# Kernel tuning notes

Measured on AMD Instinct MI355X. Metric: run time of the kernel, lower is better.

Reference implementation:

```python
import jax, jax.numpy as jnp
import numpy as np

B, T, D, U = 64, 512, 512, 512


def setup_inputs() -> dict:
    key = jax.random.key(0)
    k1, k2, k3 = jax.random.split(key, 3)
    x = jax.random.normal(k1, (B, T, D), dtype=jnp.float32)
    Wk = jax.random.normal(k2, (D, 4 * U), dtype=jnp.float32) * (1.0 / np.sqrt(D))
    Wr = jax.random.normal(k3, (U, 4 * U), dtype=jnp.float32) * (1.0 / np.sqrt(U))
    # bias init per module: zeros(i), ones(f), zeros(g), zeros(o)
    b = jnp.concatenate([jnp.zeros(U), jnp.ones(U), jnp.zeros(2 * U)]).astype(jnp.float32)
    return {"x": x, "Wk": Wk, "Wr": Wr, "b": b}


def reference(x, Wk, Wr, b):
    units = Wr.shape[0]
    # Precompute input projection for all timesteps in one GEMM (same math).
    zx = jnp.einsum('btd,dk->btk', x, Wk)  # [B, T, 4U]
    h0 = jnp.zeros((x.shape[0], units), dtype=x.dtype)
    c0 = jnp.zeros((x.shape[0], units), dtype=x.dtype)

    def step(carry, zx_t):
        h, c = carry
        z = zx_t + h @ Wr + b  # [B, 4U]
        zi, zf, zg, zo = jnp.split(z, 4, axis=-1)
        i = jax.nn.sigmoid(zi)
        f = jax.nn.sigmoid(zf)
        c_new = f * c + i * jnp.tanh(zg)
        o = jax.nn.sigmoid(zo)
        h_new = o * jnp.tanh(c_new)
        return (h_new, c_new), None

    (h_last, c_last), _ = jax.lax.scan(step, (h0, c0), jnp.swapaxes(zx, 0, 1))
    # default flags: return_sequence=False, return_states=False -> last hidden
    return h_last
```

## Files before the change

### kernel.cpp

```cpp
#include <hip/hip_runtime.h>
#include <hip/hip_bf16.h>
#include <math.h>

#define BSZ 64
#define TT  512
#define DD  512
#define UU  512
#define NZ  2048

#define NSL    32
#define USL    16
#define NBG    4
#define BG     16
#define KSTEPS 16

using short8  = __attribute__((ext_vector_type(8))) short;
using floatx4 = __attribute__((ext_vector_type(4))) float;
typedef unsigned long long u64;

template <bool ZXBF16>
__global__ __launch_bounds__(256) void gemm_zx(const float* __restrict__ A,
                                               const float* __restrict__ B,
                                               void* __restrict__ Cout) {
  __shared__ float As[16][65];
  __shared__ float Bs[16][64];

  const int tid = threadIdx.x;
  const int tx = tid & 15;
  const int ty = tid >> 4;
  const int m0 = blockIdx.y * 64;
  const int n0 = blockIdx.x * 64;

  const int lm  = tid >> 2;
  const int lk4 = (tid & 3) * 4;
  const int lk  = tid >> 4;
  const int ln4 = (tid & 15) * 4;

  float acc[4][4] = {};

  for (int k0 = 0; k0 < DD; k0 += 16) {
    float4 av = *(const float4*)(A + (size_t)(m0 + lm) * DD + k0 + lk4);
    float4 bv = *(const float4*)(B + (size_t)(k0 + lk) * NZ + n0 + ln4);
    As[lk4 + 0][lm] = av.x;
    As[lk4 + 1][lm] = av.y;
    As[lk4 + 2][lm] = av.z;
    As[lk4 + 3][lm] = av.w;
    *(float4*)&Bs[lk][ln4] = bv;
    __syncthreads();
#pragma unroll
    for (int kk = 0; kk < 16; ++kk) {
      float a[4], b[4];
#pragma unroll
      for (int i = 0; i < 4; ++i) a[i] = As[kk][ty * 4 + i];
#pragma unroll
      for (int j = 0; j < 4; ++j) b[j] = Bs[kk][tx * 4 + j];
#pragma unroll
      for (int i = 0; i < 4; ++i)
#pragma unroll
        for (int j = 0; j < 4; ++j) acc[i][j] = fmaf(a[i], b[j], acc[i][j]);
    }
    __syncthreads();
  }

#pragma unroll
  for (int i = 0; i < 4; ++i) {
    const size_t row = (size_t)(m0 + ty * 4 + i) * NZ + n0 + tx * 4;
    if constexpr (ZXBF16) {
      __hip_bfloat16* C = (__hip_bfloat16*)Cout;
#pragma unroll
      for (int j = 0; j < 4; ++j) C[row + j] = __float2bfloat16(acc[i][j]);
    } else {
      float* C = (float*)Cout;
      *(float4*)&C[row] = make_float4(acc[i][0], acc[i][1], acc[i][2], acc[i][3]);
    }
  }
}

__device__ __forceinline__ floatx4 mfma16(short8 a, short8 b, floatx4 c) {
  return __builtin_amdgcn_mfma_f32_16x16x32_bf16(a, b, c, 0, 0, 0);
}

template <bool ZXBF16>
__global__ __launch_bounds__(256) void lstm_persist(
    const void* __restrict__ zx_, const float* __restrict__ Wr,
    const float* __restrict__ bias, unsigned short* __restrict__ h_hi,
    unsigned short* __restrict__ h_lo, int* __restrict__ flags,
    float* __restrict__ out) {
  extern __shared__ char lds[];
  unsigned short* wr_hi = (unsigned short*)lds;
  unsigned short* wr_lo = wr_hi + KSTEPS * 4 * 64 * 8;
  float* z_ex = (float*)(wr_lo + KSTEPS * 4 * 64 * 8);

  const int sl = blockIdx.x;
  const int bg = blockIdx.y;
  const int tid = threadIdx.x;
  const int g = tid >> 6;
  const int lane = tid & 63;
  const int u0 = sl * USL;

  {
    const int cidx = tid & 63;
    const int koff = tid >> 6;
    const int gg = cidx >> 4, u = cidx & 15;
    const int col = gg * UU + u0 + u;
    for (int k0 = 0; k0 < DD; k0 += 4) {
      const int k = k0 + koff;
      const float v = Wr[(size_t)k * NZ + col];
      const __hip_bfloat16 vh = __float2bfloat16(v);
      const float rem = v - __bfloat162float(vh);
      const __hip_bfloat16 vl = __float2bfloat16(rem);
      const int K = k >> 5, kg = (k >> 3) & 3, j = k & 7;
      const int off = ((K * 4 + gg) * 64 + (kg * 16 + u)) * 8 + j;
      wr_hi[off] = *(const unsigned short*)&vh;
      wr_lo[off] = *(const unsigned short*)&vl;
    }
  }
  __syncthreads();

  const int am = lane & 15, akg = lane >> 4;
  const size_t arow = (size_t)(bg * BG + am) * UU + akg * 8;

  const int eb = tid >> 4;
  const int eu = tid & 15;
  const int b = bg * BG + eb;
  const float bias_i = bias[0 * UU + u0 + eu];
  const float bias_f = bias[1 * UU + u0 + eu];
  const float bias_g = bias[2 * UU + u0 + eu];
  const float bias_o = bias[3 * UU + u0 + eu];
  float c_state = 0.f;
  const size_t plane_t = (size_t)BSZ * UU;
  const int wword = (b * UU + u0 + eu) >> 1;

  int* myflag = flags + (bg * NSL + sl) * 16;

  for (int t = 0; t < TT; ++t) {
    float zi, zf, zg, zo;
    {
      const size_t zb = ((size_t)b * TT + t) * NZ + u0 + eu;
      if constexpr (ZXBF16) {
        const unsigned short* zx = (const unsigned short*)zx_;
        zi = __bfloat162float(*(const __hip_bfloat16*)&zx[zb + 0 * UU]);
        zf = __bfloat162float(*(const __hip_bfloat16*)&zx[zb + 1 * UU]);
        zg = __bfloat162float(*(const __hip_bfloat16*)&zx[zb + 2 * UU]);
        zo = __bfloat162float(*(const __hip_bfloat16*)&zx[zb + 3 * UU]);
      } else {
        const float* zx = (const float*)zx_;
        zi = zx[zb + 0 * UU];
        zf = zx[zb + 1 * UU];
        zg = zx[zb + 2 * UU];
        zo = zx[zb + 3 * UU];
      }
    }

    if (tid < NSL) {
      const int* fp = flags + (bg * NSL + tid) * 16;
      while (__hip_atomic_load(fp, __ATOMIC_RELAXED, __HIP_MEMORY_SCOPE_AGENT) < t) {
      }
    }
    __syncthreads();
    __builtin_amdgcn_fence(__ATOMIC_ACQUIRE, "workgroup");

    const unsigned short* Ahi = h_hi + (size_t)t * plane_t + arow;
    const unsigned short* Alo = h_lo + (size_t)t * plane_t + arow;
    floatx4 a0 = {0, 0, 0, 0}, a1 = {0, 0, 0, 0}, a2 = {0, 0, 0, 0};
#pragma unroll 4
    for (int K = 0; K < KSTEPS; ++K) {
      const short8 ahi = *(const short8*)(Ahi + K * 32);
      const short8 alo = *(const short8*)(Alo + K * 32);
      const short8 bhi = *(const short8*)(wr_hi + ((K * 4 + g) * 64 + lane) * 8);
      const short8 blo = *(const short8*)(wr_lo + ((K * 4 + g) * 64 + lane) * 8);
      a0 = mfma16(ahi, bhi, a0);
      a1 = mfma16(ahi, blo, a1);
      a2 = mfma16(alo, bhi, a2);
    }
#pragma unroll
    for (int r = 0; r < 4; ++r) {
      const int bb = (lane >> 4) * 4 + r;
      z_ex[(g * 16 + bb) * 16 + (lane & 15)] = a0[r] + a1[r] + a2[r];
    }
    __syncthreads();

    zi += z_ex[(0 * 16 + eb) * 16 + eu] + bias_i;
    zf += z_ex[(1 * 16 + eb) * 16 + eu] + bias_f;
    zg += z_ex[(2 * 16 + eb) * 16 + eu] + bias_g;
    zo += z_ex[(3 * 16 + eb) * 16 + eu] + bias_o;

    const float ig = 1.f / (1.f + expf(-zi));
    const float fg = 1.f / (1.f + expf(-zf));
    const float gg = tanhf(zg);
    const float og = 1.f / (1.f + expf(-zo));
    c_state = fg * c_state + ig * gg;
    const float hn = og * tanhf(c_state);

    const __hip_bfloat16 hh = __float2bfloat16(hn);
    const float hrem = hn - __bfloat162float(hh);
    const __hip_bfloat16 hl = __float2bfloat16(hrem);
    const unsigned int vhi = (unsigned int)*(const unsigned short*)&hh;
    const unsigned int vlo = (unsigned int)*(const unsigned short*)&hl;
    const unsigned int phi_n = (unsigned int)__shfl_xor((int)vhi, 1);
    const unsigned int plo_n = (unsigned int)__shfl_xor((int)vlo, 1);
    if ((tid & 1) == 0) {
      const unsigned int whi = vhi | (phi_n << 16);
      const unsigned int wlo = vlo | (plo_n << 16);
      unsigned int* phi = (unsigned int*)(h_hi + (size_t)(t + 1) * plane_t) + wword;
      unsigned int* plo = (unsigned int*)(h_lo + (size_t)(t + 1) * plane_t) + wword;
      __hip_atomic_store(phi, whi, __ATOMIC_RELAXED, __HIP_MEMORY_SCOPE_AGENT);
      __hip_atomic_store(plo, wlo, __ATOMIC_RELAXED, __HIP_MEMORY_SCOPE_AGENT);
    }

    if (t == TT - 1) out[(size_t)b * UU + u0 + eu] = hn;

    __syncthreads();
    if (tid == 0)
      __hip_atomic_store(myflag, t + 1, __ATOMIC_RELAXED,
                         __HIP_MEMORY_SCOPE_AGENT);
  }
}

extern "C" void kernel_launch(void* const* d_in, const int* in_sizes, int n_in,
                              void* d_out, int out_size, void* d_ws, size_t ws_size,
                              hipStream_t stream) {
  const float* x    = (const float*)d_in[0];
  const float* Wk   = (const float*)d_in[1];
  const float* Wr   = (const float*)d_in[2];
  const float* bias = (const float*)d_in[3];
  float* out = (float*)d_out;

  const size_t plane_t = (size_t)BSZ * UU;
  const size_t hplane_bytes = (size_t)(TT + 1) * plane_t * 2;
  const size_t flags_bytes = (size_t)NBG * NSL * 16 * 4;
  const size_t zx_f32_bytes = (size_t)BSZ * TT * NZ * 4;

  const size_t need_f32 = zx_f32_bytes + 2 * hplane_bytes + flags_bytes;
  const bool use_bf16_zx = (ws_size < need_f32);
  const size_t zx_bytes = use_bf16_zx ? zx_f32_bytes / 2 : zx_f32_bytes;

  char* ws = (char*)d_ws;
  void* zx = (void*)ws;
  unsigned short* h_hi = (unsigned short*)(ws + zx_bytes);
  unsigned short* h_lo = (unsigned short*)(ws + zx_bytes + hplane_bytes);
  int* flags = (int*)(ws + zx_bytes + 2 * hplane_bytes);

  hipMemsetAsync(h_hi, 0, plane_t * 2, stream);
  hipMemsetAsync(h_lo, 0, plane_t * 2, stream);
  hipMemsetAsync(flags, 0, flags_bytes, stream);

  dim3 ggrid(NZ / 64, (BSZ * TT) / 64);
  if (use_bf16_zx)
    gemm_zx<true><<<ggrid, 256, 0, stream>>>(x, Wk, zx);
  else
    gemm_zx<false><<<ggrid, 256, 0, stream>>>(x, Wk, zx);

  const int lds_bytes = KSTEPS * 4 * 64 * 8 * 2 * 2 + 4 * 16 * 16 * 4;
  dim3 pgrid(NSL, NBG);
  if (use_bf16_zx) {
    hipFuncSetAttribute(reinterpret_cast<const void*>(lstm_persist<true>),
                        hipFuncAttributeMaxDynamicSharedMemorySize, lds_bytes);
    lstm_persist<true><<<pgrid, 256, lds_bytes, stream>>>(zx, Wr, bias, h_hi, h_lo,
                                                          flags, out);
  } else {
    hipFuncSetAttribute(reinterpret_cast<const void*>(lstm_persist<false>),
                        hipFuncAttributeMaxDynamicSharedMemorySize, lds_bytes);
    lstm_persist<false><<<pgrid, 256, lds_bytes, stream>>>(zx, Wr, bias, h_hi, h_lo,
                                                           flags, out);
  }
}
```

Before: 4.406 ms.

## Pin LSTM batch groups to XCDs via runtime election, use plain stores locally

Splits the batch into 8 groups of 8 rows and grows the persistent grid to 256 blocks. Each block reads its hardware XCC_ID and joins an atomic election that assigns it a batch group on its own XCD, so each batch group's hidden-state exchange stays within one XCD's L2. When every XCD receives exactly 32 blocks, hidden-state writes become plain stores instead of agent-scope atomics. The cost is half-idle MFMA rows (the 16-row tile holds only 8 real rows), half the threads idle in the elementwise phase, and an all-block spin barrier at startup that assumes all 256 blocks are co-resident. Using plain stores also relies on flags and cache coherence holding within an XCD.

```diff
diff --git a/kernel.cpp b/kernel.cpp
--- a/kernel.cpp
+++ b/kernel.cpp
@@ -10,13 +10,12 @@
 
 #define NSL    32
 #define USL    16
-#define NBG    4
-#define BG     16
+#define NBG    8
+#define BG     8
 #define KSTEPS 16
 
 using short8  = __attribute__((ext_vector_type(8))) short;
 using floatx4 = __attribute__((ext_vector_type(4))) float;
-typedef unsigned long long u64;
 
 template <bool ZXBF16>
 __global__ __launch_bounds__(256) void gemm_zx(const float* __restrict__ A,
@@ -85,17 +84,62 @@
     const void* __restrict__ zx_, const float* __restrict__ Wr,
     const float* __restrict__ bias, unsigned short* __restrict__ h_hi,
     unsigned short* __restrict__ h_lo, int* __restrict__ flags,
-    float* __restrict__ out) {
+    int* __restrict__ elect, float* __restrict__ out) {
   extern __shared__ char lds[];
   unsigned short* wr_hi = (unsigned short*)lds;
   unsigned short* wr_lo = wr_hi + KSTEPS * 4 * 64 * 8;
   float* z_ex = (float*)(wr_lo + KSTEPS * 4 * 64 * 8);
-
-  const int sl = blockIdx.x;
-  const int bg = blockIdx.y;
+  int* s_meta = (int*)(z_ex + 4 * 16 * 16);
+
   const int tid = threadIdx.x;
   const int g = tid >> 6;
   const int lane = tid & 63;
+
+  if (tid == 0) {
+    int xcd;
+    asm volatile("s_getreg_b32 %0, hwreg(HW_REG_XCC_ID)" : "=s"(xcd));
+    xcd &= 7;
+    const int local = __hip_atomic_fetch_add(elect + (2 + xcd) * 16, 1,
+                                             __ATOMIC_RELAXED,
+                                             __HIP_MEMORY_SCOPE_AGENT);
+    __hip_atomic_fetch_add(elect, 1, __ATOMIC_ACQ_REL, __HIP_MEMORY_SCOPE_AGENT);
+    while (__hip_atomic_load(elect, __ATOMIC_ACQUIRE,
+                             __HIP_MEMORY_SCOPE_AGENT) < 256) {
+    }
+    int cnt[8];
+    bool even = true;
+    for (int j = 0; j < 8; ++j) {
+      cnt[j] = __hip_atomic_load(elect + (2 + j) * 16, __ATOMIC_RELAXED,
+                                 __HIP_MEMORY_SCOPE_AGENT);
+      even = even && (cnt[j] == 32);
+    }
+    int bg, sl;
+    if (local < 32) {
+      bg = xcd;
+      sl = local;
+    } else {
+      int k = __hip_atomic_fetch_add(elect + 16, 1, __ATOMIC_RELAXED,
+                                     __HIP_MEMORY_SCOPE_AGENT);
+      bg = 0;
+      sl = 0;
+      for (int j = 0; j < 8; ++j) {
+        const int d = cnt[j] < 32 ? 32 - cnt[j] : 0;
+        if (k < d) {
+          bg = j;
+          sl = cnt[j] + k;
+          break;
+        }
+        k -= d;
+      }
+    }
+    s_meta[0] = bg;
+    s_meta[1] = sl;
+    s_meta[2] = even ? 1 : 0;
+  }
+  __syncthreads();
+  const int bg = s_meta[0];
+  const int sl = s_meta[1];
+  const bool local_mode = s_meta[2] != 0;
   const int u0 = sl * USL;
 
   {
@@ -118,7 +162,7 @@
   __syncthreads();
 
   const int am = lane & 15, akg = lane >> 4;
-  const size_t arow = (size_t)(bg * BG + am) * UU + akg * 8;
+  const size_t arow = (size_t)(am & 7) * UU + akg * 8;
 
   const int eb = tid >> 4;
   const int eu = tid & 15;
@@ -128,14 +172,14 @@
   const float bias_g = bias[2 * UU + u0 + eu];
   const float bias_o = bias[3 * UU + u0 + eu];
   float c_state = 0.f;
-  const size_t plane_t = (size_t)BSZ * UU;
-  const int wword = (b * UU + u0 + eu) >> 1;
+  const size_t plane_t = (size_t)NBG * BG * UU;
+  const int wword_loc = (eb * UU + u0 + eu) >> 1;
 
   int* myflag = flags + (bg * NSL + sl) * 16;
 
   for (int t = 0; t < TT; ++t) {
-    float zi, zf, zg, zo;
-    {
+    float zi = 0.f, zf = 0.f, zg = 0.f, zo = 0.f;
+    if (tid < 128) {
       const size_t zb = ((size_t)b * TT + t) * NZ + u0 + eu;
       if constexpr (ZXBF16) {
         const unsigned short* zx = (const unsigned short*)zx_;
@@ -160,8 +204,10 @@
     __syncthreads();
     __builtin_amdgcn_fence(__ATOMIC_ACQUIRE, "workgroup");
 
-    const unsigned short* Ahi = h_hi + (size_t)t * plane_t + arow;
-    const unsigned short* Alo = h_lo + (size_t)t * plane_t + arow;
+    const unsigned short* Ahi =
+        h_hi + ((size_t)t * NBG + bg) * (BG * UU) + arow;
+    const unsigned short* Alo =
+        h_lo + ((size_t)t * NBG + bg) * (BG * UU) + arow;
     floatx4 a0 = {0, 0, 0, 0}, a1 = {0, 0, 0, 0}, a2 = {0, 0, 0, 0};
 #pragma unroll 4
     for (int K = 0; K < KSTEPS; ++K) {
@@ -175,40 +221,47 @@
     }
 #pragma unroll
     for (int r = 0; r < 4; ++r) {
-      const int bb = (lane >> 4) * 4 + r;
-      z_ex[(g * 16 + bb) * 16 + (lane & 15)] = a0[r] + a1[r] + a2[r];
-    }
-    __syncthreads();
-
-    zi += z_ex[(0 * 16 + eb) * 16 + eu] + bias_i;
-    zf += z_ex[(1 * 16 + eb) * 16 + eu] + bias_f;
-    zg += z_ex[(2 * 16 + eb) * 16 + eu] + bias_g;
-    zo += z_ex[(3 * 16 + eb) * 16 + eu] + bias_o;
-
-    const float ig = 1.f / (1.f + expf(-zi));
-    const float fg = 1.f / (1.f + expf(-zf));
-    const float gg = tanhf(zg);
-    const float og = 1.f / (1.f + expf(-zo));
-    c_state = fg * c_state + ig * gg;
-    const float hn = og * tanhf(c_state);
-
-    const __hip_bfloat16 hh = __float2bfloat16(hn);
-    const float hrem = hn - __bfloat162float(hh);
-    const __hip_bfloat16 hl = __float2bfloat16(hrem);
-    const unsigned int vhi = (unsigned int)*(const unsigned short*)&hh;
-    const unsigned int vlo = (unsigned int)*(const unsigned short*)&hl;
-    const unsigned int phi_n = (unsigned int)__shfl_xor((int)vhi, 1);
-    const unsigned int plo_n = (unsigned int)__shfl_xor((int)vlo, 1);
-    if ((tid & 1) == 0) {
-      const unsigned int whi = vhi | (phi_n << 16);
-      const unsigned int wlo = vlo | (plo_n << 16);
-      unsigned int* phi = (unsigned int*)(h_hi + (size_t)(t + 1) * plane_t) + wword;
-      unsigned int* plo = (unsigned int*)(h_lo + (size_t)(t + 1) * plane_t) + wword;
-      __hip_atomic_store(phi, whi, __ATOMIC_RELAXED, __HIP_MEMORY_SCOPE_AGENT);
-      __hip_atomic_store(plo, wlo, __ATOMIC_RELAXED, __HIP_MEMORY_SCOPE_AGENT);
-    }
-
-    if (t == TT - 1) out[(size_t)b * UU + u0 + eu] = hn;
+      const int rr = (lane >> 4) * 4 + r;
+      z_ex[(g * 16 + rr) * 16 + (lane & 15)] = a0[r] + a1[r] + a2[r];
+    }
+    __syncthreads();
+
+    if (tid < 128) {
+      zi += z_ex[(0 * 16 + eb) * 16 + eu] + bias_i;
+      zf += z_ex[(1 * 16 + eb) * 16 + eu] + bias_f;
+      zg += z_ex[(2 * 16 + eb) * 16 + eu] + bias_g;
+      zo += z_ex[(3 * 16 + eb) * 16 + eu] + bias_o;
+
+      const float ig = 1.f / (1.f + expf(-zi));
+      const float fg = 1.f / (1.f + expf(-zf));
+      const float gg = tanhf(zg);
+      const float og = 1.f / (1.f + expf(-zo));
+      c_state = fg * c_state + ig * gg;
+      const float hn = og * tanhf(c_state);
+
+      const __hip_bfloat16 hh = __float2bfloat16(hn);
+      const float hrem = hn - __bfloat162float(hh);
+      const __hip_bfloat16 hl = __float2bfloat16(hrem);
+      const unsigned int vhi = (unsigned int)*(const unsigned short*)&hh;
+      const unsigned int vlo = (unsigned int)*(const unsigned short*)&hl;
+      const unsigned int nhi = (unsigned int)__shfl_xor((int)vhi, 1);
+      const unsigned int nlo = (unsigned int)__shfl_xor((int)vlo, 1);
+      if ((eu & 1) == 0) {
+        const unsigned int whi = vhi | (nhi << 16);
+        const unsigned int wlo = vlo | (nlo << 16);
+        const size_t wbase = ((size_t)(t + 1) * NBG + bg) * (BG * UU / 2);
+        unsigned int* phi = (unsigned int*)h_hi + wbase + wword_loc;
+        unsigned int* plo = (unsigned int*)h_lo + wbase + wword_loc;
+        if (local_mode) {
+          *phi = whi;
+          *plo = wlo;
+        } else {
+          __hip_atomic_store(phi, whi, __ATOMIC_RELAXED, __HIP_MEMORY_SCOPE_AGENT);
+          __hip_atomic_store(plo, wlo, __ATOMIC_RELAXED, __HIP_MEMORY_SCOPE_AGENT);
+        }
+      }
+      if (t == TT - 1) out[(size_t)b * UU + u0 + eu] = hn;
+    }
 
     __syncthreads();
     if (tid == 0)
@@ -226,12 +279,14 @@
   const float* bias = (const float*)d_in[3];
   float* out = (float*)d_out;
 
-  const size_t plane_t = (size_t)BSZ * UU;
+  const size_t plane_t = (size_t)NBG * BG * UU;
   const size_t hplane_bytes = (size_t)(TT + 1) * plane_t * 2;
   const size_t flags_bytes = (size_t)NBG * NSL * 16 * 4;
+  const size_t elect_bytes = (size_t)(2 + 8) * 16 * 4;
   const size_t zx_f32_bytes = (size_t)BSZ * TT * NZ * 4;
 
-  const size_t need_f32 = zx_f32_bytes + 2 * hplane_bytes + flags_bytes;
+  const size_t need_f32 =
+      zx_f32_bytes + 2 * hplane_bytes + flags_bytes + elect_bytes;
   const bool use_bf16_zx = (ws_size < need_f32);
   const size_t zx_bytes = use_bf16_zx ? zx_f32_bytes / 2 : zx_f32_bytes;
 
@@ -240,10 +295,12 @@
   unsigned short* h_hi = (unsigned short*)(ws + zx_bytes);
   unsigned short* h_lo = (unsigned short*)(ws + zx_bytes + hplane_bytes);
   int* flags = (int*)(ws + zx_bytes + 2 * hplane_bytes);
+  int* elect = (int*)(ws + zx_bytes + 2 * hplane_bytes + flags_bytes);
 
   hipMemsetAsync(h_hi, 0, plane_t * 2, stream);
   hipMemsetAsync(h_lo, 0, plane_t * 2, stream);
   hipMemsetAsync(flags, 0, flags_bytes, stream);
+  hipMemsetAsync(elect, 0, elect_bytes, stream);
 
   dim3 ggrid(NZ / 64, (BSZ * TT) / 64);
   if (use_bf16_zx)
@@ -251,17 +308,16 @@
   else
     gemm_zx<false><<<ggrid, 256, 0, stream>>>(x, Wk, zx);
 
-  const int lds_bytes = KSTEPS * 4 * 64 * 8 * 2 * 2 + 4 * 16 * 16 * 4;
-  dim3 pgrid(NSL, NBG);
+  const int lds_bytes = KSTEPS * 4 * 64 * 8 * 2 * 2 + 4 * 16 * 16 * 4 + 64;
   if (use_bf16_zx) {
     hipFuncSetAttribute(reinterpret_cast<const void*>(lstm_persist<true>),
                         hipFuncAttributeMaxDynamicSharedMemorySize, lds_bytes);
-    lstm_persist<true><<<pgrid, 256, lds_bytes, stream>>>(zx, Wr, bias, h_hi, h_lo,
-                                                          flags, out);
+    lstm_persist<true><<<256, 256, lds_bytes, stream>>>(zx, Wr, bias, h_hi, h_lo,
+                                                        flags, elect, out);
   } else {
     hipFuncSetAttribute(reinterpret_cast<const void*>(lstm_persist<false>),
                         hipFuncAttributeMaxDynamicSharedMemorySize, lds_bytes);
-    lstm_persist<false><<<pgrid, 256, lds_bytes, stream>>>(zx, Wr, bias, h_hi, h_lo,
-                                                           flags, out);
+    lstm_persist<false><<<256, 256, lds_bytes, stream>>>(zx, Wr, bias, h_hi, h_lo,
+                                                         flags, elect, out);
   }
 }
```

New measurement: 5.168 ms. +17.3%, slower.
